# Kernel optimization log

Measured on AMD Instinct MI355X. Metric: run time of the kernel, lower is better.

The kernel has to match this reference:

```python
import jax, jax.numpy as jnp
import numpy as np

N, E, F_IN, E_DIM, H, G = 8192, 40960, 32, 8, 64, 64
EPS = 1e-5


def _lin(key, fan_in, fan_out):
    k1, k2 = jax.random.split(key)
    s = 1.0 / np.sqrt(fan_in)
    w = jax.random.uniform(k1, (fan_in, fan_out), jnp.float32, -s, s)
    b = jax.random.uniform(k2, (fan_out,), jnp.float32, -s, s)
    return w, b


def setup_inputs() -> dict:
    key = jax.random.key(0)
    ks = jax.random.split(key, 32)
    inp = {}
    inp['x'] = jax.random.normal(ks[0], (N, F_IN), jnp.float32)
    inp['edge_index'] = jax.random.randint(ks[1], (2, E), 0, N)
    inp['edge_attr'] = jax.random.normal(ks[2], (E, E_DIM), jnp.float32)
    inp['batch'] = jnp.sort(jax.random.randint(ks[3], (N,), 0, G))
    # NNConv 1 (F_IN -> H)
    inp['e1_w1'], inp['e1_b1'] = _lin(ks[4], E_DIM, H)
    inp['e1_w2'], inp['e1_b2'] = _lin(ks[5], H, F_IN * H)
    inp['root1_w'], inp['root1_b'] = _lin(ks[6], F_IN, H)
    inp['bn1_g'] = jnp.ones((H,), jnp.float32); inp['bn1_b'] = jnp.zeros((H,), jnp.float32)
    # NNConv 2 (H -> H)
    inp['e2_w1'], inp['e2_b1'] = _lin(ks[7], E_DIM, H)
    inp['e2_w2'], inp['e2_b2'] = _lin(ks[8], H, H * H)
    inp['root2_w'], inp['root2_b'] = _lin(ks[9], H, H)
    inp['bn2_g'] = jnp.ones((H,), jnp.float32); inp['bn2_b'] = jnp.zeros((H,), jnp.float32)
    # NNConv 3 (H -> H)
    inp['e3_w1'], inp['e3_b1'] = _lin(ks[10], E_DIM, H)
    inp['e3_w2'], inp['e3_b2'] = _lin(ks[11], H, H * H)
    inp['root3_w'], inp['root3_b'] = _lin(ks[12], H, H)
    inp['bn3_g'] = jnp.ones((H,), jnp.float32); inp['bn3_b'] = jnp.zeros((H,), jnp.float32)
    # attention gate MLP: H -> H//2 -> 1
    inp['gate_w1'], inp['gate_b1'] = _lin(ks[13], H, H // 2)
    inp['gate_w2'], inp['gate_b2'] = _lin(ks[14], H // 2, 1)
    # fc head: H -> 2H (BN, relu) -> H (BN, relu) -> 1
    inp['fc1_w'], inp['fc1_b'] = _lin(ks[15], H, 2 * H)
    inp['fcbn1_g'] = jnp.ones((2 * H,), jnp.float32); inp['fcbn1_b'] = jnp.zeros((2 * H,), jnp.float32)
    inp['fc2_w'], inp['fc2_b'] = _lin(ks[16], 2 * H, H)
    inp['fcbn2_g'] = jnp.ones((H,), jnp.float32); inp['fcbn2_b'] = jnp.zeros((H,), jnp.float32)
    inp['fc3_w'], inp['fc3_b'] = _lin(ks[17], H, 1)
    return inp


def _bn(x, g, b):
    # training-mode batch norm over node/graph dim
    m = jnp.mean(x, axis=0)
    v = jnp.var(x, axis=0)
    return (x - m) * jax.lax.rsqrt(v + EPS) * g + b


def _nnconv(x, edge_index, edge_attr, w1, b1, w2, b2, root_w, root_b, in_ch, out_ch):
    src, dst = edge_index[0], edge_index[1]
    h = jax.nn.relu(edge_attr @ w1 + b1)                     # [E, H]
    We = (h @ w2 + b2).reshape(-1, in_ch, out_ch)            # [E, in, out]
    msg = jnp.einsum('ei,eio->eo', x[src], We)               # [E, out]
    s = jax.ops.segment_sum(msg, dst, num_segments=N)
    cnt = jax.ops.segment_sum(jnp.ones((msg.shape[0],), x.dtype), dst, num_segments=N)
    agg = s / jnp.clip(cnt, 1.0)[:, None]                    # mean aggregation
    return agg + x @ root_w + root_b


def _global_attention(x, batch, gw1, gb1, gw2, gb2):
    gate = jax.nn.relu(x @ gw1 + gb1) @ gw2 + gb2            # [N, 1]
    gate = gate[:, 0]
    m = jax.ops.segment_max(gate, batch, num_segments=G)
    e = jnp.exp(gate - m[batch])
    z = jax.ops.segment_sum(e, batch, num_segments=G)
    alpha = e / z[batch]
    return jax.ops.segment_sum(alpha[:, None] * x, batch, num_segments=G)  # [G, H]


def reference(x, edge_index, edge_attr, batch,
              e1_w1, e1_b1, e1_w2, e1_b2, root1_w, root1_b, bn1_g, bn1_b,
              e2_w1, e2_b1, e2_w2, e2_b2, root2_w, root2_b, bn2_g, bn2_b,
              e3_w1, e3_b1, e3_w2, e3_b2, root3_w, root3_b, bn3_g, bn3_b,
              gate_w1, gate_b1, gate_w2, gate_b2,
              fc1_w, fc1_b, fcbn1_g, fcbn1_b, fc2_w, fc2_b, fcbn2_g, fcbn2_b, fc3_w, fc3_b):
    x1 = jax.nn.relu(_bn(_nnconv(x, edge_index, edge_attr, e1_w1, e1_b1, e1_w2, e1_b2, root1_w, root1_b, F_IN, H), bn1_g, bn1_b))
    x2 = jax.nn.relu(_bn(_nnconv(x1, edge_index, edge_attr, e2_w1, e2_b1, e2_w2, e2_b2, root2_w, root2_b, H, H), bn2_g, bn2_b)) + x1
    x3 = jax.nn.relu(_bn(_nnconv(x2, edge_index, edge_attr, e3_w1, e3_b1, e3_w2, e3_b2, root3_w, root3_b, H, H), bn3_g, bn3_b)) + x2
    # dropout is identity in eval/reference mode
    p = _global_attention(x3, batch, gate_w1, gate_b1, gate_w2, gate_b2)  # [G, H]
    h = jax.nn.relu(_bn(p @ fc1_w + fc1_b, fcbn1_g, fcbn1_b))
    h = jax.nn.relu(_bn(h @ fc2_w + fc2_b, fcbn2_g, fcbn2_b))
    out = h @ fc3_w + fc3_b
    return out[:, 0]
```

## Files before the change

### kernel.cpp

```cpp
#include <hip/hip_runtime.h>
#include <hip/hip_bf16.h>

#define NN 8192
#define EE 40960
#define FIN 32
#define HH 64
#define GG 64

typedef __attribute__((ext_vector_type(4))) float f32x4;
typedef __attribute__((ext_vector_type(8))) short s16x8;
typedef unsigned short ushort_t;

__device__ __forceinline__ unsigned short f2bf(float f) {
    union { float f; unsigned int u; } v; v.f = f;
    unsigned int u = v.u;
    return (unsigned short)((u + 0x7fffu + ((u >> 16) & 1u)) >> 16);
}

__device__ __forceinline__ void gll16(const void* g, void* l) {
    __builtin_amdgcn_global_load_lds((__attribute__((address_space(1))) void*)g,
                                     (__attribute__((address_space(3))) void*)l, 16, 0, 0);
}

__global__ void btbuild_all_kernel(const float* __restrict__ w2a, const float* __restrict__ b2a, ushort_t* __restrict__ Bta,
                                   const float* __restrict__ w2b, const float* __restrict__ b2b, ushort_t* __restrict__ Btb,
                                   const float* __restrict__ w2c, const float* __restrict__ b2c, ushort_t* __restrict__ Btc,
                                   int* __restrict__ cnt, int* __restrict__ fill, float* __restrict__ stats) {
    int bid = blockIdx.x;
    int t = threadIdx.x;
    if (bid < 32) { cnt[bid * 256 + t] = 0; fill[bid * 256 + t] = 0; }
    if (bid == 32) stats[t] = 0.f;
    if (bid == 33 && t < 128) stats[256 + t] = 0.f;

    const float* w2; const float* b2; ushort_t* Bt; int IC; int base;
    if (bid < 520)       { w2 = w2a; b2 = b2a; Bt = Bta; IC = 32; base = bid; }
    else if (bid < 1560) { w2 = w2b; b2 = b2b; Bt = Btb; IC = 64; base = bid - 520; }
    else                 { w2 = w2c; b2 = b2c; Bt = Btc; IC = 64; base = bid - 1560; }
    int CH = IC >> 3;
    int flat = base * 256 + t;
    if (flat >= 64 * 65 * IC) return;
    int s = flat / (64 * IC);
    int rem = flat - s * (64 * IC);
    int row = rem / IC;
    int j = rem - row * IC;
    int q = j >> 3, w = j & 7;
    int c = q ^ (row & (CH - 1));
    int i = c * 8 + w;
    float v = (s < 64) ? w2[s * (IC * 64) + i * 64 + row] : b2[i * 64 + row];
    Bt[flat] = f2bf(v);
}

__global__ void hist_kernel(const int* __restrict__ dst, int* __restrict__ cnt) {
    int e = blockIdx.x * 256 + threadIdx.x;
    if (e < EE) atomicAdd(&cnt[dst[e]], 1);
}

__global__ void scan_kernel(const int* __restrict__ cnt, int* __restrict__ row_ptr) {
    __shared__ int lds[1024];
    int t = threadIdx.x;
    int v[8]; int s = 0;
    int base = t * 8;
#pragma unroll
    for (int j = 0; j < 8; j++) { v[j] = s; s += cnt[base + j]; }
    lds[t] = s;
    __syncthreads();
    for (int off = 1; off < 1024; off <<= 1) {
        int add = (t >= off) ? lds[t - off] : 0;
        __syncthreads();
        lds[t] += add;
        __syncthreads();
    }
    int ex = lds[t] - s;
#pragma unroll
    for (int j = 0; j < 8; j++) row_ptr[base + j] = ex + v[j];
    if (t == 1023) row_ptr[NN] = lds[1023];
}

__global__ void scatter_kernel(const int* __restrict__ dst, const int* __restrict__ row_ptr,
                               int* __restrict__ fill, int* __restrict__ perm) {
    int e = blockIdx.x * 256 + threadIdx.x;
    if (e < EE) {
        int d = dst[e];
        int pos = row_ptr[d] + atomicAdd(&fill[d], 1);
        perm[pos] = e;
    }
}

template<int IC>
__launch_bounds__(256, 4)
__global__ void conv_msg_kernel(const float* __restrict__ eattr,
                                const float* __restrict__ w1,
                                const float* __restrict__ b1,
                                const float* __restrict__ xin,
                                const int* __restrict__ src,
                                const int* __restrict__ perm,
                                const ushort_t* __restrict__ Bt,
                                float* __restrict__ msg) {
    constexpr int NKK  = IC / 32;
    constexpr int CH   = IC / 8;
    constexpr int TILE = IC * 64;
    constexpr int WT   = IC * 16;
    constexpr int NQ   = (WT * 2) / 1024;
    __shared__ ushort_t bt_lds[4][4][WT];
    __shared__ float h_t[4096];
    __shared__ float ea_s[64][9];
    __shared__ float w1s[512];
    __shared__ float b1s[64];
    __shared__ int eid_s[64];

    const int t = threadIdx.x;
    const int wave = t >> 6;
    const int l = t & 63;
    const int g = l >> 4;
    const int rlo = l & 15;
    const int e0 = blockIdx.x * 64;

    if (t < 64) { eid_s[t] = perm[e0 + t]; b1s[t] = b1[t]; }
    for (int i = t; i < 512; i += 256) w1s[i] = w1[i];
    __syncthreads();

#pragma unroll
    for (int j = 0; j < 2; j++) {
        int idx = t + 256 * j;
        int e = idx >> 3, i = idx & 7;
        ea_s[e][i] = eattr[(size_t)eid_s[e] * 8 + i];
    }

    s16x8 afrag[4][NKK];
#pragma unroll
    for (int m = 0; m < 4; ++m) {
        int row = m * 16 + rlo;
        int sn = src[eid_s[row]];
        const float* xp = xin + (size_t)sn * IC + g * 8;
#pragma unroll
        for (int kk = 0; kk < NKK; ++kk) {
            f32x4 a = *(const f32x4*)(xp + kk * 32);
            f32x4 b = *(const f32x4*)(xp + kk * 32 + 4);
            s16x8 fr;
            fr[0] = (short)f2bf(a[0]); fr[1] = (short)f2bf(a[1]);
            fr[2] = (short)f2bf(a[2]); fr[3] = (short)f2bf(a[3]);
            fr[4] = (short)f2bf(b[0]); fr[5] = (short)f2bf(b[1]);
            fr[6] = (short)f2bf(b[2]); fr[7] = (short)f2bf(b[3]);
            afrag[m][kk] = fr;
        }
    }
    __syncthreads();

#pragma unroll
    for (int j = 0; j < 16; ++j) {
        int k = wave * 16 + j;
        float s = b1s[k];
#pragma unroll
        for (int i = 0; i < 8; i++) s += ea_s[l][i] * w1s[i * 64 + k];
        h_t[(k << 6) + l] = fmaxf(s, 0.f);
    }
    __syncthreads();

    auto stage = [&](int step) {
        int s2 = step > 64 ? 64 : step;
        ushort_t* lp = &bt_lds[step & 3][wave][0];
        const ushort_t* gp = Bt + (size_t)s2 * TILE + wave * WT + l * 8;
        gll16(gp, lp);
        if constexpr (NQ == 2) gll16(gp + 512, lp + 512);
    };

    stage(0); stage(1); stage(2);

    f32x4 acc[4];
#pragma unroll
    for (int m = 0; m < 4; m++) acc[m] = (f32x4){0.f, 0.f, 0.f, 0.f};

    const int bmask = rlo & (CH - 1);
    const f32x4 zf = (f32x4){0.f, 0.f, 0.f, 0.f};

    for (int step = 0; step < 65; ++step) {
        if constexpr (NQ == 2) asm volatile("s_waitcnt vmcnt(4)" ::: "memory");
        else                   asm volatile("s_waitcnt vmcnt(2)" ::: "memory");
        __builtin_amdgcn_sched_barrier(0);
        const ushort_t* wbuf = &bt_lds[step & 3][wave][0];
        s16x8 bfr[NKK];
#pragma unroll
        for (int kk = 0; kk < NKK; kk++) {
            int q = (kk * 4 + g) ^ bmask;
            bfr[kk] = *(const s16x8*)&wbuf[rlo * IC + q * 8];
        }
#pragma unroll
        for (int m = 0; m < 4; m++) {
            f32x4 P = __builtin_amdgcn_mfma_f32_16x16x32_bf16(afrag[m][0], bfr[0], zf, 0, 0, 0);
            if constexpr (NKK == 2)
                P = __builtin_amdgcn_mfma_f32_16x16x32_bf16(afrag[m][1], bfr[1], P, 0, 0, 0);
            if (step == 64) {
                acc[m] += P;
            } else {
                f32x4 h4 = *(const f32x4*)&h_t[(step << 6) + m * 16 + (g << 2)];
                acc[m] += h4 * P;
            }
        }
        stage(step + 3);
    }

#pragma unroll
    for (int m = 0; m < 4; m++) {
        int row = e0 + m * 16 + (g << 2);
        float* mp = msg + (size_t)row * 64 + wave * 16 + rlo;
        mp[0] = acc[m][0]; mp[64] = acc[m][1]; mp[128] = acc[m][2]; mp[192] = acc[m][3];
    }
}

__global__ void aggregate_kernel(const float* __restrict__ msg, const int* __restrict__ row_ptr,
                                 const float* __restrict__ xin, int IC,
                                 const float* __restrict__ root_w, const float* __restrict__ root_b,
                                 float* __restrict__ y, float* __restrict__ stats) {
    int t = threadIdx.x;
    int n = blockIdx.x * 16 + (t >> 4);
    int cg = (t & 15) * 4;
    int s = row_ptr[n], e = row_ptr[n + 1];
    f32x4 acc = (f32x4){0.f, 0.f, 0.f, 0.f};
    for (int j = s; j < e; ++j) {
        acc += *(const f32x4*)&msg[(size_t)j * 64 + cg];
    }
    float inv = 1.0f / fmaxf((float)(e - s), 1.0f);
    acc *= inv;
    const float* xr = xin + (size_t)n * IC;
    for (int i = 0; i < IC; ++i) {
        float xv = xr[i];
        acc += xv * (*(const f32x4*)&root_w[i * 64 + cg]);
    }
    acc += *(const f32x4*)&root_b[cg];
    *(f32x4*)&y[(size_t)n * 64 + cg] = acc;

    f32x4 a2 = acc * acc;
#pragma unroll
    for (int j = 0; j < 4; j++) {
        acc[j] += __shfl_xor(acc[j], 16); acc[j] += __shfl_xor(acc[j], 32);
        a2[j]  += __shfl_xor(a2[j], 16);  a2[j]  += __shfl_xor(a2[j], 32);
    }
    __shared__ float ls[4][64], lq[4][64];
    int w = t >> 6;
    if ((t & 63) < 16) {
#pragma unroll
        for (int j = 0; j < 4; j++) { ls[w][cg + j] = acc[j]; lq[w][cg + j] = a2[j]; }
    }
    __syncthreads();
    if (t < 64) {
        float S = ls[0][t] + ls[1][t] + ls[2][t] + ls[3][t];
        float Q = lq[0][t] + lq[1][t] + lq[2][t] + lq[3][t];
        atomicAdd(&stats[t], S);
        atomicAdd(&stats[64 + t], Q);
    }
}

__global__ void bn_apply_kernel(const float* __restrict__ y, const float* __restrict__ stats,
                                const float* __restrict__ gam, const float* __restrict__ bet,
                                const float* __restrict__ res, float* __restrict__ xout) {
    int i4 = blockIdx.x * 256 + threadIdx.x;
    int cg = (i4 & 15) * 4;
    const float invN = 1.0f / (float)NN;
    f32x4 yv = *(const f32x4*)&y[(size_t)i4 * 4];
    f32x4 o;
#pragma unroll
    for (int j = 0; j < 4; j++) {
        int c = cg + j;
        float mean = stats[c] * invN;
        float var = stats[64 + c] * invN - mean * mean;
        float sc = rsqrtf(var + 1e-5f) * gam[c];
        float v = (yv[j] - mean) * sc + bet[c];
        o[j] = fmaxf(v, 0.f);
    }
    if (res) o += *(const f32x4*)&res[(size_t)i4 * 4];
    *(f32x4*)&xout[(size_t)i4 * 4] = o;
}

__global__ void bn_gate_kernel(const float* __restrict__ y, const float* __restrict__ stats,
                               const float* __restrict__ gam, const float* __restrict__ bet,
                               const float* __restrict__ res, float* __restrict__ xout,
                               const float* __restrict__ gw1, const float* __restrict__ gb1,
                               const float* __restrict__ gw2, const float* __restrict__ gb2,
                               float* __restrict__ gate) {
    __shared__ float x3s[64][68];
    __shared__ float w1s[2048];
    __shared__ float b1s[32], w2s[32];
    __shared__ float b2s;
    int t = threadIdx.x;
    for (int i = t; i < 2048; i += 256) w1s[i] = gw1[i];
    if (t < 32) { b1s[t] = gb1[t]; w2s[t] = gw2[t]; }
    if (t == 0) b2s = gb2[0];
    const float invN = 1.0f / (float)NN;
    size_t base4 = (size_t)blockIdx.x * 1024;
#pragma unroll
    for (int j = 0; j < 4; j++) {
        int i4l = j * 256 + t;
        int row = i4l >> 4, cg = (i4l & 15) * 4;
        f32x4 yv = *(const f32x4*)&y[(base4 + i4l) * 4];
        f32x4 o;
#pragma unroll
        for (int jj = 0; jj < 4; jj++) {
            int c = cg + jj;
            float mean = stats[c] * invN;
            float var = stats[64 + c] * invN - mean * mean;
            float sc = rsqrtf(var + 1e-5f) * gam[c];
            o[jj] = fmaxf((yv[jj] - mean) * sc + bet[c], 0.f);
        }
        o += *(const f32x4*)&res[(base4 + i4l) * 4];
        *(f32x4*)&xout[(base4 + i4l) * 4] = o;
        *(f32x4*)&x3s[row][cg] = o;
    }
    __syncthreads();
    int w = t >> 6, l = t & 63;
    int row = w * 16 + (l >> 2), part = l & 3;
    float hacc[8];
#pragma unroll
    for (int j = 0; j < 8; j++) hacc[j] = b1s[part * 8 + j];
    for (int i = 0; i < 64; i++) {
        float xv = x3s[row][i];
#pragma unroll
        for (int j = 0; j < 8; j++) hacc[j] += xv * w1s[i * 32 + part * 8 + j];
    }
    float gv = 0.f;
#pragma unroll
    for (int j = 0; j < 8; j++) gv += fmaxf(hacc[j], 0.f) * w2s[part * 8 + j];
    gv += __shfl_xor(gv, 1); gv += __shfl_xor(gv, 2);
    if (part == 0) gate[blockIdx.x * 64 + row] = gv + b2s;
}

__global__ void attn_pool_kernel(const float* __restrict__ x3, const float* __restrict__ gate,
                                 const int* __restrict__ batch, float* __restrict__ p) {
    int g = blockIdx.x;
    int t = threadIdx.x;
    int lo = 0, hi = NN;
    while (lo < hi) { int mid = (lo + hi) >> 1; if (batch[mid] < g) lo = mid + 1; else hi = mid; }
    int s = lo;
    hi = NN;
    while (lo < hi) { int mid = (lo + hi) >> 1; if (batch[mid] < g + 1) lo = mid + 1; else hi = mid; }
    int e = lo;

    __shared__ float red[4];
    __shared__ float sM, sZ;
    float m = -1e30f;
    for (int n = s + t; n < e; n += 256) m = fmaxf(m, gate[n]);
#pragma unroll
    for (int off = 1; off < 64; off <<= 1) m = fmaxf(m, __shfl_xor(m, off));
    if ((t & 63) == 0) red[t >> 6] = m;
    __syncthreads();
    if (t == 0) sM = fmaxf(fmaxf(red[0], red[1]), fmaxf(red[2], red[3]));
    __syncthreads();
    float z = 0.f;
    for (int n = s + t; n < e; n += 256) z += __expf(gate[n] - sM);
#pragma unroll
    for (int off = 1; off < 64; off <<= 1) z += __shfl_xor(z, off);
    if ((t & 63) == 0) red[t >> 6] = z;
    __syncthreads();
    if (t == 0) sZ = red[0] + red[1] + red[2] + red[3];
    __syncthreads();
    int w = t >> 6, c = t & 63;
    float acc = 0.f;
    for (int n = s + w; n < e; n += 4) acc += __expf(gate[n] - sM) * x3[(size_t)n * 64 + c];
    __shared__ float pa[4][64];
    pa[w][c] = acc;
    __syncthreads();
    if (t < 64) {
        float v = pa[0][t] + pa[1][t] + pa[2][t] + pa[3][t];
        p[g * 64 + t] = (sZ > 0.f) ? v / sZ : 0.f;
    }
}

__global__ void head1_kernel(const float* __restrict__ p, const float* __restrict__ fc1w,
                             const float* __restrict__ fc1b, const float* __restrict__ bn1g,
                             const float* __restrict__ bn1b, float* __restrict__ t1n) {
    __shared__ float sp[64 * 65];
    __shared__ float w1s[64 * 16];
    __shared__ float t1s[64 * 17];
    __shared__ float sA[16], sB[16];
    int t = threadIdx.x;
    int c0 = blockIdx.x * 16;
    for (int i = t; i < 4096; i += 256) { int r = i >> 6, cc = i & 63; sp[r * 65 + cc] = p[i]; }
    for (int i = t; i < 1024; i += 256) { int r = i >> 4, cc = i & 15; w1s[i] = fc1w[r * 128 + c0 + cc]; }
    __syncthreads();
    int r16 = t >> 4, c = t & 15;
    float b = fc1b[c0 + c];
#pragma unroll
    for (int rb = 0; rb < 4; rb++) {
        int row = rb * 16 + r16;
        float s = b;
#pragma unroll 8
        for (int i = 0; i < 64; i++) s += sp[row * 65 + i] * w1s[i * 16 + c];
        t1s[row * 17 + c] = s;
    }
    __syncthreads();
    if (t < 16) {
        float su = 0.f, sq = 0.f;
        for (int r = 0; r < 64; r++) { float v = t1s[r * 17 + t]; su += v; sq += v * v; }
        float mean = su * (1.f / 64.f), var = sq * (1.f / 64.f) - mean * mean;
        float sc = rsqrtf(var + 1e-5f) * bn1g[c0 + t];
        sA[t] = sc; sB[t] = bn1b[c0 + t] - mean * sc;
    }
    __syncthreads();
#pragma unroll
    for (int rb = 0; rb < 4; rb++) {
        int row = rb * 16 + r16;
        float v = t1s[row * 17 + c] * sA[c] + sB[c];
        t1n[row * 128 + c0 + c] = fmaxf(v, 0.f);
    }
}

__global__ void head2_kernel(const float* __restrict__ t1n, const float* __restrict__ fc2w,
                             const float* __restrict__ fc2b, const float* __restrict__ bn2g,
                             const float* __restrict__ bn2b, float* __restrict__ y2n) {
    __shared__ float t1sh[64 * 129];
    __shared__ float w2s[128 * 8];
    __shared__ float t2s[64 * 9];
    __shared__ float sA[8], sB[8];
    int t = threadIdx.x;
    int c0 = blockIdx.x * 8;
    for (int i = t; i < 8192; i += 256) { int r = i >> 7, cc = i & 127; t1sh[r * 129 + cc] = t1n[i]; }
    for (int i = t; i < 1024; i += 256) { int r = i >> 3, cc = i & 7; w2s[i] = fc2w[r * 64 + c0 + cc]; }
    __syncthreads();
    int r32 = t >> 3, c = t & 7;
    float b = fc2b[c0 + c];
#pragma unroll
    for (int rb = 0; rb < 2; rb++) {
        int row = rb * 32 + r32;
        float s = b;
#pragma unroll 8
        for (int i = 0; i < 128; i++) s += t1sh[row * 129 + i] * w2s[i * 8 + c];
        t2s[row * 9 + c] = s;
    }
    __syncthreads();
    if (t < 8) {
        float su = 0.f, sq = 0.f;
        for (int r = 0; r < 64; r++) { float v = t2s[r * 9 + t]; su += v; sq += v * v; }
        float mean = su * (1.f / 64.f), var = sq * (1.f / 64.f) - mean * mean;
        float sc = rsqrtf(var + 1e-5f) * bn2g[c0 + t];
        sA[t] = sc; sB[t] = bn2b[c0 + t] - mean * sc;
    }
    __syncthreads();
#pragma unroll
    for (int rb = 0; rb < 2; rb++) {
        int row = rb * 32 + r32;
        float v = t2s[row * 9 + c] * sA[c] + sB[c];
        y2n[row * 64 + c0 + c] = fmaxf(v, 0.f);
    }
}

__global__ void head3_kernel(const float* __restrict__ y2n, const float* __restrict__ fc3w,
                             const float* __restrict__ fc3b, float* __restrict__ out) {
    __shared__ float w3[64];
    int t = threadIdx.x;
    w3[t] = fc3w[t];
    __syncthreads();
    float s = fc3b[0];
    const float* yr = y2n + t * 64;
#pragma unroll 8
    for (int i = 0; i < 64; i++) s += yr[i] * w3[i];
    out[t] = s;
}

extern "C" void kernel_launch(void* const* d_in, const int* in_sizes, int n_in,
                              void* d_out, int out_size, void* d_ws, size_t ws_size,
                              hipStream_t stream) {
    const float* x     = (const float*)d_in[0];
    const int*   eidx  = (const int*)d_in[1];
    const float* eattr = (const float*)d_in[2];
    const int*   batch = (const int*)d_in[3];
    const float* e1w1 = (const float*)d_in[4];  const float* e1b1 = (const float*)d_in[5];
    const float* e1w2 = (const float*)d_in[6];  const float* e1b2 = (const float*)d_in[7];
    const float* r1w  = (const float*)d_in[8];  const float* r1b  = (const float*)d_in[9];
    const float* bn1g = (const float*)d_in[10]; const float* bn1b = (const float*)d_in[11];
    const float* e2w1 = (const float*)d_in[12]; const float* e2b1 = (const float*)d_in[13];
    const float* e2w2 = (const float*)d_in[14]; const float* e2b2 = (const float*)d_in[15];
    const float* r2w  = (const float*)d_in[16]; const float* r2b  = (const float*)d_in[17];
    const float* bn2g = (const float*)d_in[18]; const float* bn2b = (const float*)d_in[19];
    const float* e3w1 = (const float*)d_in[20]; const float* e3b1 = (const float*)d_in[21];
    const float* e3w2 = (const float*)d_in[22]; const float* e3b2 = (const float*)d_in[23];
    const float* r3w  = (const float*)d_in[24]; const float* r3b  = (const float*)d_in[25];
    const float* bn3g = (const float*)d_in[26]; const float* bn3b = (const float*)d_in[27];
    const float* gw1  = (const float*)d_in[28]; const float* gb1  = (const float*)d_in[29];
    const float* gw2  = (const float*)d_in[30]; const float* gb2  = (const float*)d_in[31];
    const float* fc1w = (const float*)d_in[32]; const float* fc1b = (const float*)d_in[33];
    const float* fbn1g= (const float*)d_in[34]; const float* fbn1b= (const float*)d_in[35];
    const float* fc2w = (const float*)d_in[36]; const float* fc2b = (const float*)d_in[37];
    const float* fbn2g= (const float*)d_in[38]; const float* fbn2b= (const float*)d_in[39];
    const float* fc3w = (const float*)d_in[40]; const float* fc3b = (const float*)d_in[41];
    float* out = (float*)d_out;

    const int* src = eidx;
    const int* dst = eidx + EE;

    char* ws = (char*)d_ws;
    size_t off = 0;
    auto take = [&](size_t n) { void* p = ws + off; off = (off + n + 255) & ~(size_t)255; return p; };
    ushort_t* Bt1 = (ushort_t*)take(64 * 2080 * 2 + 256);
    ushort_t* Bt2 = (ushort_t*)take(64 * 4160 * 2 + 256);
    ushort_t* Bt3 = (ushort_t*)take(64 * 4160 * 2 + 256);
    float* msg  = (float*)take((size_t)EE * 64 * 4);
    float* ybuf = (float*)take((size_t)NN * 64 * 4);
    float* x1   = (float*)take((size_t)NN * 64 * 4);
    float* x2   = (float*)take((size_t)NN * 64 * 4);
    float* x3   = (float*)take((size_t)NN * 64 * 4);
    float* gate = (float*)take((size_t)NN * 4);
    float* pbuf = (float*)take(64 * 64 * 4);
    float* t1n  = (float*)take(64 * 128 * 4);
    float* y2n  = (float*)take(64 * 64 * 4);
    float* stats = (float*)take(384 * 4);
    int* cnt  = (int*)take((size_t)NN * 4);
    int* fill = (int*)take((size_t)NN * 4);
    int* rowp = (int*)take((size_t)(NN + 1) * 4);
    int* perm = (int*)take((size_t)EE * 4);

    btbuild_all_kernel<<<2600, 256, 0, stream>>>(e1w2, e1b2, Bt1, e2w2, e2b2, Bt2,
                                                 e3w2, e3b2, Bt3, cnt, fill, stats);
    hist_kernel<<<160, 256, 0, stream>>>(dst, cnt);
    scan_kernel<<<1, 1024, 0, stream>>>(cnt, rowp);
    scatter_kernel<<<160, 256, 0, stream>>>(dst, rowp, fill, perm);

    conv_msg_kernel<32><<<640, 256, 0, stream>>>(eattr, e1w1, e1b1, x, src, perm, Bt1, msg);
    aggregate_kernel<<<512, 256, 0, stream>>>(msg, rowp, x, 32, r1w, r1b, ybuf, stats);
    bn_apply_kernel<<<512, 256, 0, stream>>>(ybuf, stats, bn1g, bn1b, nullptr, x1);

    conv_msg_kernel<64><<<640, 256, 0, stream>>>(eattr, e2w1, e2b1, x1, src, perm, Bt2, msg);
    aggregate_kernel<<<512, 256, 0, stream>>>(msg, rowp, x1, 64, r2w, r2b, ybuf, stats + 128);
    bn_apply_kernel<<<512, 256, 0, stream>>>(ybuf, stats + 128, bn2g, bn2b, x1, x2);

    conv_msg_kernel<64><<<640, 256, 0, stream>>>(eattr, e3w1, e3b1, x2, src, perm, Bt3, msg);
    aggregate_kernel<<<512, 256, 0, stream>>>(msg, rowp, x2, 64, r3w, r3b, ybuf, stats + 256);
    bn_gate_kernel<<<128, 256, 0, stream>>>(ybuf, stats + 256, bn3g, bn3b, x2, x3,
                                            gw1, gb1, gw2, gb2, gate);

    attn_pool_kernel<<<64, 256, 0, stream>>>(x3, gate, batch, pbuf);
    head1_kernel<<<8, 256, 0, stream>>>(pbuf, fc1w, fc1b, fbn1g, fbn1b, t1n);
    head2_kernel<<<8, 256, 0, stream>>>(t1n, fc2w, fc2b, fbn2g, fbn2b, y2n);
    head3_kernel<<<1, 64, 0, stream>>>(y2n, fc3w, fc3b, out);
}
```

Before: 264.2 us.

## Load B fragments directly into registers instead of staging through LDS

Each wave's per-step B-tile fragments are now read straight into VGPRs with inline global_load_dwordx4, replacing the global_load_lds staging through a 4-deep LDS ring. The loop is manually unrolled by four with rotating register buffers, and the final bias step is peeled off the loop. The XOR swizzle in the Bt build is dropped because LDS bank conflicts no longer apply. This removes the LDS traffic and LDS footprint, which may improve occupancy, at the cost of more VGPRs. The last three issued loads read past the 65 valid tiles into extra padded workspace that is never used.

```diff
diff --git a/kernel.cpp b/kernel.cpp
--- a/kernel.cpp
+++ b/kernel.cpp
@@ -17,11 +17,6 @@
     return (unsigned short)((u + 0x7fffu + ((u >> 16) & 1u)) >> 16);
 }
 
-__device__ __forceinline__ void gll16(const void* g, void* l) {
-    __builtin_amdgcn_global_load_lds((__attribute__((address_space(1))) void*)g,
-                                     (__attribute__((address_space(3))) void*)l, 16, 0, 0);
-}
-
 __global__ void btbuild_all_kernel(const float* __restrict__ w2a, const float* __restrict__ b2a, ushort_t* __restrict__ Bta,
                                    const float* __restrict__ w2b, const float* __restrict__ b2b, ushort_t* __restrict__ Btb,
                                    const float* __restrict__ w2c, const float* __restrict__ b2c, ushort_t* __restrict__ Btc,
@@ -36,16 +31,12 @@
     if (bid < 520)       { w2 = w2a; b2 = b2a; Bt = Bta; IC = 32; base = bid; }
     else if (bid < 1560) { w2 = w2b; b2 = b2b; Bt = Btb; IC = 64; base = bid - 520; }
     else                 { w2 = w2c; b2 = b2c; Bt = Btc; IC = 64; base = bid - 1560; }
-    int CH = IC >> 3;
     int flat = base * 256 + t;
     if (flat >= 64 * 65 * IC) return;
     int s = flat / (64 * IC);
     int rem = flat - s * (64 * IC);
     int row = rem / IC;
-    int j = rem - row * IC;
-    int q = j >> 3, w = j & 7;
-    int c = q ^ (row & (CH - 1));
-    int i = c * 8 + w;
+    int i = rem - row * IC;
     float v = (s < 64) ? w2[s * (IC * 64) + i * 64 + row] : b2[i * 64 + row];
     Bt[flat] = f2bf(v);
 }
@@ -97,11 +88,7 @@
                                 const ushort_t* __restrict__ Bt,
                                 float* __restrict__ msg) {
     constexpr int NKK  = IC / 32;
-    constexpr int CH   = IC / 8;
     constexpr int TILE = IC * 64;
-    constexpr int WT   = IC * 16;
-    constexpr int NQ   = (WT * 2) / 1024;
-    __shared__ ushort_t bt_lds[4][4][WT];
     __shared__ float h_t[4096];
     __shared__ float ea_s[64][9];
     __shared__ float w1s[512];
@@ -156,47 +143,74 @@
     }
     __syncthreads();
 
-    auto stage = [&](int step) {
-        int s2 = step > 64 ? 64 : step;
-        ushort_t* lp = &bt_lds[step & 3][wave][0];
-        const ushort_t* gp = Bt + (size_t)s2 * TILE + wave * WT + l * 8;
-        gll16(gp, lp);
-        if constexpr (NQ == 2) gll16(gp + 512, lp + 512);
+    const ushort_t* lane_base = Bt + (size_t)((wave * 16 + rlo) * IC + g * 8);
+    const ushort_t* p0 = lane_base;
+    const ushort_t* p1 = lane_base + TILE;
+    const ushort_t* p2 = lane_base + 2 * TILE;
+    const ushort_t* p3 = lane_base + 3 * TILE;
+
+    s16x8 b0a, b0b, b1a, b1b, b2a, b2b, b3a, b3b;
+
+    auto issue = [&](const ushort_t*& p, s16x8& da, s16x8& db) {
+        asm volatile("global_load_dwordx4 %0, %1, off" : "=v"(da) : "v"(p));
+        if constexpr (NKK == 2)
+            asm volatile("global_load_dwordx4 %0, %1, off offset:64" : "=v"(db) : "v"(p));
+        p += 4 * TILE;
     };
 
-    stage(0); stage(1); stage(2);
+    issue(p0, b0a, b0b);
+    issue(p1, b1a, b1b);
+    issue(p2, b2a, b2b);
 
     f32x4 acc[4];
 #pragma unroll
     for (int m = 0; m < 4; m++) acc[m] = (f32x4){0.f, 0.f, 0.f, 0.f};
-
-    const int bmask = rlo & (CH - 1);
     const f32x4 zf = (f32x4){0.f, 0.f, 0.f, 0.f};
 
-    for (int step = 0; step < 65; ++step) {
-        if constexpr (NQ == 2) asm volatile("s_waitcnt vmcnt(4)" ::: "memory");
-        else                   asm volatile("s_waitcnt vmcnt(2)" ::: "memory");
+    auto STEP = [&](int step, const s16x8& ba, const s16x8& bb,
+                    const ushort_t*& pn, s16x8& na, s16x8& nb) {
+        if constexpr (NKK == 2) asm volatile("s_waitcnt vmcnt(4)" ::: "memory");
+        else                    asm volatile("s_waitcnt vmcnt(2)" ::: "memory");
         __builtin_amdgcn_sched_barrier(0);
-        const ushort_t* wbuf = &bt_lds[step & 3][wave][0];
-        s16x8 bfr[NKK];
-#pragma unroll
-        for (int kk = 0; kk < NKK; kk++) {
-            int q = (kk * 4 + g) ^ bmask;
-            bfr[kk] = *(const s16x8*)&wbuf[rlo * IC + q * 8];
+        f32x4 P0 = __builtin_amdgcn_mfma_f32_16x16x32_bf16(afrag[0][0], ba, zf, 0, 0, 0);
+        f32x4 P1 = __builtin_amdgcn_mfma_f32_16x16x32_bf16(afrag[1][0], ba, zf, 0, 0, 0);
+        f32x4 P2 = __builtin_amdgcn_mfma_f32_16x16x32_bf16(afrag[2][0], ba, zf, 0, 0, 0);
+        f32x4 P3 = __builtin_amdgcn_mfma_f32_16x16x32_bf16(afrag[3][0], ba, zf, 0, 0, 0);
+        if constexpr (NKK == 2) {
+            P0 = __builtin_amdgcn_mfma_f32_16x16x32_bf16(afrag[0][1], bb, P0, 0, 0, 0);
+            P1 = __builtin_amdgcn_mfma_f32_16x16x32_bf16(afrag[1][1], bb, P1, 0, 0, 0);
+            P2 = __builtin_amdgcn_mfma_f32_16x16x32_bf16(afrag[2][1], bb, P2, 0, 0, 0);
+            P3 = __builtin_amdgcn_mfma_f32_16x16x32_bf16(afrag[3][1], bb, P3, 0, 0, 0);
         }
-#pragma unroll
-        for (int m = 0; m < 4; m++) {
-            f32x4 P = __builtin_amdgcn_mfma_f32_16x16x32_bf16(afrag[m][0], bfr[0], zf, 0, 0, 0);
-            if constexpr (NKK == 2)
-                P = __builtin_amdgcn_mfma_f32_16x16x32_bf16(afrag[m][1], bfr[1], P, 0, 0, 0);
-            if (step == 64) {
-                acc[m] += P;
-            } else {
-                f32x4 h4 = *(const f32x4*)&h_t[(step << 6) + m * 16 + (g << 2)];
-                acc[m] += h4 * P;
-            }
-        }
-        stage(step + 3);
+        const unsigned hb = (unsigned)(step << 6) + (unsigned)(g << 2);
+        f32x4 h0 = *(const f32x4*)&h_t[hb];
+        f32x4 h1 = *(const f32x4*)&h_t[hb + 16];
+        f32x4 h2 = *(const f32x4*)&h_t[hb + 32];
+        f32x4 h3 = *(const f32x4*)&h_t[hb + 48];
+        acc[0] += h0 * P0;
+        acc[1] += h1 * P1;
+        acc[2] += h2 * P2;
+        acc[3] += h3 * P3;
+        issue(pn, na, nb);
+    };
+
+    for (int blk = 0; blk < 16; ++blk) {
+        int s = blk * 4;
+        STEP(s + 0, b0a, b0b, p3, b3a, b3b);
+        STEP(s + 1, b1a, b1b, p0, b0a, b0b);
+        STEP(s + 2, b2a, b2b, p1, b1a, b1b);
+        STEP(s + 3, b3a, b3b, p2, b2a, b2b);
+    }
+
+    if constexpr (NKK == 2) asm volatile("s_waitcnt vmcnt(4)" ::: "memory");
+    else                    asm volatile("s_waitcnt vmcnt(2)" ::: "memory");
+    __builtin_amdgcn_sched_barrier(0);
+#pragma unroll
+    for (int m = 0; m < 4; m++) {
+        f32x4 P = __builtin_amdgcn_mfma_f32_16x16x32_bf16(afrag[m][0], b0a, zf, 0, 0, 0);
+        if constexpr (NKK == 2)
+            P = __builtin_amdgcn_mfma_f32_16x16x32_bf16(afrag[m][1], b0b, P, 0, 0, 0);
+        acc[m] += P;
     }
 
 #pragma unroll
@@ -489,9 +503,9 @@
     char* ws = (char*)d_ws;
     size_t off = 0;
     auto take = [&](size_t n) { void* p = ws + off; off = (off + n + 255) & ~(size_t)255; return p; };
-    ushort_t* Bt1 = (ushort_t*)take(64 * 2080 * 2 + 256);
-    ushort_t* Bt2 = (ushort_t*)take(64 * 4160 * 2 + 256);
-    ushort_t* Bt3 = (ushort_t*)take(64 * 4160 * 2 + 256);
+    ushort_t* Bt1 = (ushort_t*)take((size_t)(65 + 3) * 2048 * 2);
+    ushort_t* Bt2 = (ushort_t*)take((size_t)(65 + 3) * 4096 * 2);
+    ushort_t* Bt3 = (ushort_t*)take((size_t)(65 + 3) * 4096 * 2);
     float* msg  = (float*)take((size_t)EE * 64 * 4);
     float* ybuf = (float*)take((size_t)NN * 64 * 4);
     float* x1   = (float*)take((size_t)NN * 64 * 4);
```

Measured after the change: 287.0 us. +8.7%, slower.
